# Performance work log

Measured on AMD Instinct MI355X. Metric: run time of the kernel, lower is better.

Reference implementation:

```python
import jax, jax.numpy as jnp
import numpy as np

N_ENVS = 8
MIN_SIGMA = 0.01

def setup_inputs() -> dict:
    key = jax.random.key(0)
    ks = jax.random.split(key, 16)
    B, T, d, L, H = 32, 64, 128, 64, 256
    H2 = H // 2
    s = 0.05
    return {
        "z_signal": jax.random.normal(ks[0], (B, T, d, L), dtype=jnp.float32),
        "z_corrupt": jax.random.normal(ks[1], (B, T, d, L), dtype=jnp.float32),
        "A": jax.random.uniform(ks[2], (d, d), dtype=jnp.float32),
        "regime": jax.random.randint(ks[3], (B,), 0, N_ENVS),
        # signal_proj: Linear(L -> H)
        "W_sig": jax.random.normal(ks[4], (L, H), dtype=jnp.float32) * s,
        "b_sig": jnp.zeros((H,), dtype=jnp.float32),
        # per-env mechanisms: Linear(H->H), ReLU, Linear(H->2), stacked over envs
        "W1e": jax.random.normal(ks[5], (N_ENVS, H, H), dtype=jnp.float32) * s,
        "b1e": jnp.zeros((N_ENVS, H), dtype=jnp.float32),
        "W2e": jax.random.normal(ks[6], (N_ENVS, H, 2), dtype=jnp.float32) * s,
        "b2e": jnp.zeros((N_ENVS, 2), dtype=jnp.float32),
        # corrupt path: Linear(L -> H//2), ReLU, Linear(H//2 -> 1)
        "Wc": jax.random.normal(ks[7], (L, H2), dtype=jnp.float32) * s,
        "bc": jnp.zeros((H2,), dtype=jnp.float32),
        "Wo": jax.random.normal(ks[8], (H2, 1), dtype=jnp.float32) * s,
        "bo": jnp.zeros((1,), dtype=jnp.float32),
    }

def reference(z_signal, z_corrupt, A, regime, W_sig, b_sig, W1e, b1e, W2e, b2e, Wc, bc, Wo, bo):
    # z_signal: [B,T,d,L], A: [d,d]
    # z_agg[b,t,i,l] = sum_j A[j,i] * z_signal[b,t,j,l]  (A^T @ z per slice)
    z_agg = jnp.einsum('ji,btjl->btil', A, z_signal)
    h_signal = jnp.einsum('btdl,lh->btdh', z_agg, W_sig) + b_sig  # [B,T,d,H]

    # env dispatch: e_idx = regime if regime < n_envs else 0 (per batch element)
    eidx = jnp.where(regime >= N_ENVS, 0, regime)
    W1 = W1e[eidx]  # [B,H,H]
    b1 = b1e[eidx]  # [B,H]
    W2 = W2e[eidx]  # [B,H,2]
    b2 = b2e[eidx]  # [B,2]

    h1 = jax.nn.relu(jnp.einsum('btdh,bhk->btdk', h_signal, W1) + b1[:, None, None, :])
    out = jnp.einsum('btdh,bhk->btdk', h1, W2) + b2[:, None, None, :]  # [B,T,d,2]
    mu = out[..., 0]
    sigma = jax.nn.softplus(out[..., 1]) + MIN_SIGMA

    # corrupt contribution
    h_c = jnp.einsum('btdl,lh->btdh', z_corrupt, Wc) + bc
    contrib = (jnp.einsum('btdh,ho->btdo', jax.nn.relu(h_c), Wo) + bo)[..., 0]  # [B,T,d]
    mu = mu + contrib
    return mu, sigma
```

## Files before the change

### kernel.cpp

```cpp
#include <hip/hip_runtime.h>


typedef __attribute__((ext_vector_type(8))) short short8;
typedef __attribute__((ext_vector_type(4))) float f32x4;

#define MFMA16(a, b, c) __builtin_amdgcn_mfma_f32_16x16x32_bf16((a), (b), (c), 0, 0, 0)

__device__ __forceinline__ unsigned short f2bf(float f) {
  union { float f; unsigned u; } v; v.f = f;
  unsigned r = v.u + 0x7fffu + ((v.u >> 16) & 1u);
  return (unsigned short)(r >> 16);
}

__device__ __forceinline__ void gload16(const void* gsrc, void* ldsdst) {
  __builtin_amdgcn_global_load_lds(
      (const __attribute__((address_space(1))) unsigned int*)gsrc,
      (__attribute__((address_space(3))) unsigned int*)ldsdst, 16, 0, 0);
}

__global__ void setup_k(const float* __restrict__ A, const float* __restrict__ W_sig,
                        const float* __restrict__ b_sig, const float* __restrict__ W1e,
                        const float* __restrict__ b1e, const float* __restrict__ W2e,
                        const float* __restrict__ Wc,
                        unsigned short* __restrict__ wsw1s, unsigned short* __restrict__ at_f,
                        unsigned short* __restrict__ wct_f, float* __restrict__ bw) {
  int blk = blockIdx.x, tid = threadIdx.x;
  if (blk < 512) {
    int e = blk >> 6, l = blk & 63, h = tid;
    const float* w1 = W1e + e * 65536 + h;
    const float* ws = W_sig + l * 256;
    float acc = 0.f;
    #pragma unroll 8
    for (int h1 = 0; h1 < 256; ++h1) acc = fmaf(ws[h1], w1[h1 * 256], acc);
    int c = h >> 7, hh = h & 127, gl = l >> 3, e8 = l & 7;
    wsw1s[((e * 2 + c) * 128 + hh) * 64 + ((gl ^ (hh & 7)) << 3) + e8] = f2bf(acc);
  } else if (blk < 576) {
    int idx = (blk - 512) * 256 + tid;
    int frag = idx >> 3, e8 = idx & 7;
    int it = frag >> 8, ks = (frag >> 6) & 3, lane = frag & 63;
    int j = ks * 32 + (lane >> 4) * 8 + e8, i = it * 16 + (lane & 15);
    at_f[idx] = f2bf(A[j * 128 + i]);
  } else if (blk < 608) {
    int idx = (blk - 576) * 256 + tid;
    int frag = idx >> 3, e8 = idx & 7;
    int ht = frag >> 7, ks = (frag >> 6) & 1, lane = frag & 63;
    int l = ks * 32 + (lane >> 4) * 8 + e8, h = ht * 16 + (lane & 15);
    wct_f[idx] = f2bf(Wc[l * 128 + h]);
  } else if (blk < 624) {
    int idx = (blk - 608) * 256 + tid;
    int e = idx >> 9, r = idx & 511;
    bw[e * 768 + 256 + r] = W2e[idx];
  } else {
    int e = blk - 624, h = tid;
    const float* w1 = W1e + e * 65536 + h;
    float acc = b1e[e * 256 + h];
    for (int h1 = 0; h1 < 256; ++h1) acc = fmaf(b_sig[h1], w1[h1 * 256], acc);
    bw[e * 768 + h] = acc;
  }
}

__global__ __launch_bounds__(256, 3) void dec_k(
    const float* __restrict__ zs, const float* __restrict__ zcr,
    const int* __restrict__ regime, const float* __restrict__ b2e,
    const float* __restrict__ bc, const float* __restrict__ Wo,
    const float* __restrict__ bo,
    const unsigned short* __restrict__ wsw1s, const unsigned short* __restrict__ at_f,
    const unsigned short* __restrict__ wct_f, const float* __restrict__ bw,
    float* __restrict__ out) {
  __shared__ __align__(16) char sm[54272];
  float* s_bias1 = (float*)(sm + 49152);
  float* s_W2    = s_bias1 + 256;
  float* s_cpart = (float*)(sm + 52224);

  const int bt = ((blockIdx.x & 7) << 8) | (blockIdx.x >> 3);
  const int tid = threadIdx.x;
  const int lane = tid & 63, wave = tid >> 6, lg = lane >> 4, l15 = lane & 15;
  int e = regime[bt >> 6]; if (e >= 8) e = 0;
  const float b2_0 = b2e[2 * e], b2_1 = b2e[2 * e + 1], bo0 = bo[0];

  const float* Z  = zs  + (size_t)bt * 8192;
  const float* Zc = zcr + (size_t)bt * 8192;
  const unsigned short* wse = wsw1s + (size_t)e * 16384;

  #pragma unroll
  for (int k = 0; k < 4; ++k)
    gload16((const char*)wse + (k * 256 + tid) * 16,
            sm + 32768 + (k * 256 + wave * 64) * 16);
  if (wave < 3)
    gload16((const char*)(bw + e * 768) + tid * 16, sm + 49152 + wave * 1024);

  float4 zcv[8];
  #pragma unroll
  for (int k = 0; k < 8; ++k) {
    int g = k * 256 + tid, d = g >> 4, l0 = (g & 15) * 4;
    zcv[k] = *(const float4*)(Zc + d * 64 + l0);
  }
  float4 z0v[4], z1v[4];
  #pragma unroll
  for (int k = 0; k < 4; ++k) {
    int g = k * 256 + tid, j = (g >> 4) * 2, l0 = (g & 15) * 4;
    const float* p = Z + j * 64 + l0;
    z0v[k] = *(const float4*)p;
    z1v[k] = *(const float4*)(p + 64);
  }
  short8 wfr[2][2];
  #pragma unroll
  for (int m = 0; m < 2; ++m)
    #pragma unroll
    for (int ks = 0; ks < 2; ++ks)
      wfr[m][ks] = *(const short8*)(wct_f + ((((wave * 2 + m) * 2 + ks) * 64 + lane) << 3));

  #pragma unroll
  for (int k = 0; k < 8; ++k) {
    int g = k * 256 + tid, d = g >> 4, l0 = (g & 15) * 4;
    unsigned lo = (unsigned)f2bf(zcv[k].x) | ((unsigned)f2bf(zcv[k].y) << 16);
    unsigned hi = (unsigned)f2bf(zcv[k].z) | ((unsigned)f2bf(zcv[k].w) << 16);
    int a = (d * 128 + l0 * 2) ^ ((d & 7) << 4);
    *(unsigned long long*)(sm + 16384 + a) = ((unsigned long long)hi << 32) | lo;
  }
  #pragma unroll
  for (int k = 0; k < 4; ++k) {
    int g = k * 256 + tid, j = (g >> 4) * 2, l0 = (g & 15) * 4;
    float a0[4] = {z0v[k].x, z0v[k].y, z0v[k].z, z0v[k].w};
    float a1[4] = {z1v[k].x, z1v[k].y, z1v[k].z, z1v[k].w};
    #pragma unroll
    for (int i2 = 0; i2 < 4; ++i2) {
      int l = l0 + i2;
      unsigned v = (unsigned)f2bf(a0[i2]) | ((unsigned)f2bf(a1[i2]) << 16);
      int a = (l * 256 + j * 2) ^ ((((l >> 2) ^ l) & 7) << 4);
      *(unsigned*)(sm + a) = v;
    }
  }
  __syncthreads();

  short8 abfr[2][4];
  #pragma unroll
  for (int m = 0; m < 2; ++m)
    #pragma unroll
    for (int ks = 0; ks < 4; ++ks)
      abfr[m][ks] = *(const short8*)(at_f + ((((wave * 2 + m) * 4 + ks) * 64 + lane) << 3));
  float4 bcv[2], wov[2];
  #pragma unroll
  for (int m = 0; m < 2; ++m) {
    int hb = (wave * 2 + m) * 16 + lg * 4;
    bcv[m] = *(const float4*)(bc + hb);
    wov[m] = *(const float4*)(Wo + hb);
  }

  float cp[8];
  #pragma unroll
  for (int dt = 0; dt < 8; ++dt) cp[dt] = 0.f;
  #pragma unroll
  for (int dt = 0; dt < 8; ++dt) {
    int brow = dt * 16 + l15;
    short8 bfr0 = *(const short8*)(sm + 16384 + ((brow * 128 + lg * 16) ^ ((brow & 7) << 4)));
    short8 bfr1 = *(const short8*)(sm + 16384 + ((brow * 128 + lg * 16 + 64) ^ ((brow & 7) << 4)));
    #pragma unroll
    for (int m = 0; m < 2; ++m) {
      f32x4 acc = (f32x4){0.f, 0.f, 0.f, 0.f};
      acc = MFMA16(wfr[m][0], bfr0, acc);
      acc = MFMA16(wfr[m][1], bfr1, acc);
      #pragma unroll
      for (int r = 0; r < 4; ++r)
        cp[dt] += fmaxf(acc[r] + bcv[m][r], 0.f) * wov[m][r];
    }
  }
  #pragma unroll
  for (int dt = 0; dt < 8; ++dt) {
    cp[dt] += __shfl_xor(cp[dt], 16);
    cp[dt] += __shfl_xor(cp[dt], 32);
  }
  if (lane < 16) {
    #pragma unroll
    for (int dt = 0; dt < 8; ++dt)
      s_cpart[wave * 128 + dt * 16 + lane] = cp[dt];
  }

  f32x4 acc1[4][2];
  #pragma unroll
  for (int lt = 0; lt < 4; ++lt)
    #pragma unroll
    for (int m = 0; m < 2; ++m) acc1[lt][m] = (f32x4){0.f, 0.f, 0.f, 0.f};
  #pragma unroll
  for (int ks = 0; ks < 4; ++ks) {
    #pragma unroll
    for (int lt = 0; lt < 4; ++lt) {
      int arow = lt * 16 + l15;
      short8 afr = *(const short8*)(sm + ((arow * 256 + lg * 16 + ks * 64) ^
                                          ((((arow >> 2) ^ arow) & 7) << 4)));
      #pragma unroll
      for (int m = 0; m < 2; ++m) acc1[lt][m] = MFMA16(afr, abfr[m][ks], acc1[lt][m]);
    }
  }
  __syncthreads();

  #pragma unroll
  for (int k = 0; k < 4; ++k)
    gload16((const char*)wse + 16384 + (k * 256 + tid) * 16,
            sm + (k * 256 + wave * 64) * 16);

  #pragma unroll
  for (int lt = 0; lt < 4; ++lt) {
    int l0 = lt * 16 + lg * 4;
    #pragma unroll
    for (int m = 0; m < 2; ++m) {
      int i = (wave * 2 + m) * 16 + l15;
      unsigned lo = (unsigned)f2bf(acc1[lt][m][0]) | ((unsigned)f2bf(acc1[lt][m][1]) << 16);
      unsigned hi = (unsigned)f2bf(acc1[lt][m][2]) | ((unsigned)f2bf(acc1[lt][m][3]) << 16);
      int a = (i * 128 + l0 * 2) ^ ((i & 7) << 4);
      *(unsigned long long*)(sm + 16384 + a) = ((unsigned long long)hi << 32) | lo;
    }
  }
  short8 mbfr[2][2];
  #pragma unroll
  for (int m = 0; m < 2; ++m) {
    int brow = (wave * 2 + m) * 16 + l15;
    #pragma unroll
    for (int ks = 0; ks < 2; ++ks)
      mbfr[m][ks] = *(const short8*)(sm + 16384 +
                       ((brow * 128 + lg * 16 + ks * 64) ^ ((brow & 7) << 4)));
  }

  float v0[2] = {0.f, 0.f}, v1[2] = {0.f, 0.f};
  #pragma unroll
  for (int c = 0; c < 2; ++c) {
    if (c == 1) __syncthreads();
    const char* wbase = (const char*)sm + (c == 0 ? 32768 : 0);
    #pragma unroll
    for (int ht = 0; ht < 8; ++ht) {
      int arow = ht * 16 + l15;
      int h4 = c * 128 + ht * 16 + lg * 4;
      short8 wa0 = *(const short8*)(wbase + ((arow * 128 + lg * 16) ^ ((arow & 7) << 4)));
      short8 wa1 = *(const short8*)(wbase + ((arow * 128 + lg * 16 + 64) ^ ((arow & 7) << 4)));
      float4 b1v = *(const float4*)(s_bias1 + h4);
      float4 w2a = *(const float4*)(s_W2 + h4 * 2);
      float4 w2b = *(const float4*)(s_W2 + h4 * 2 + 4);
      #pragma unroll
      for (int m = 0; m < 2; ++m) {
        f32x4 acc = (f32x4){0.f, 0.f, 0.f, 0.f};
        acc = MFMA16(wa0, mbfr[m][0], acc);
        acc = MFMA16(wa1, mbfr[m][1], acc);
        float p0 = fmaxf(acc[0] + b1v.x, 0.f), p1 = fmaxf(acc[1] + b1v.y, 0.f);
        float p2 = fmaxf(acc[2] + b1v.z, 0.f), p3 = fmaxf(acc[3] + b1v.w, 0.f);
        v0[m] = fmaf(p0, w2a.x, fmaf(p1, w2a.z, fmaf(p2, w2b.x, fmaf(p3, w2b.z, v0[m]))));
        v1[m] = fmaf(p0, w2a.y, fmaf(p1, w2a.w, fmaf(p2, w2b.y, fmaf(p3, w2b.w, v1[m]))));
      }
    }
  }
  #pragma unroll
  for (int m = 0; m < 2; ++m) {
    v0[m] += __shfl_xor(v0[m], 16); v0[m] += __shfl_xor(v0[m], 32);
    v1[m] += __shfl_xor(v1[m], 16); v1[m] += __shfl_xor(v1[m], 32);
  }
  if (lane < 16) {
    #pragma unroll
    for (int m = 0; m < 2; ++m) {
      int d = (wave * 2 + m) * 16 + lane;
      float contrib = s_cpart[d] + s_cpart[128 + d] + s_cpart[256 + d] + s_cpart[384 + d];
      float mu = v0[m] + b2_0 + bo0 + contrib;
      float x = v1[m] + b2_1;
      float sg = fmaxf(x, 0.f) + log1pf(expf(-fabsf(x))) + 0.01f;
      out[(size_t)bt * 128 + d] = mu;
      out[262144 + (size_t)bt * 128 + d] = sg;
    }
  }
}

extern "C" void kernel_launch(void* const* d_in, const int* in_sizes, int n_in,
                              void* d_out, int out_size, void* d_ws, size_t ws_size,
                              hipStream_t stream) {
  const float* zs    = (const float*)d_in[0];
  const float* zcr   = (const float*)d_in[1];
  const float* A     = (const float*)d_in[2];
  const int*   reg   = (const int*)d_in[3];
  const float* W_sig = (const float*)d_in[4];
  const float* b_sig = (const float*)d_in[5];
  const float* W1e   = (const float*)d_in[6];
  const float* b1e   = (const float*)d_in[7];
  const float* W2e   = (const float*)d_in[8];
  const float* b2e   = (const float*)d_in[9];
  const float* Wc    = (const float*)d_in[10];
  const float* bcp   = (const float*)d_in[11];
  const float* Wo    = (const float*)d_in[12];
  const float* bo    = (const float*)d_in[13];

  unsigned short* wsw1s = (unsigned short*)d_ws;
  unsigned short* at_f  = wsw1s + 131072;
  unsigned short* wct_f = at_f + 16384;
  float* bw             = (float*)(wct_f + 8192);

  setup_k<<<632, 256, 0, stream>>>(A, W_sig, b_sig, W1e, b1e, W2e, Wc,
                                   wsw1s, at_f, wct_f, bw);
  dec_k<<<2048, 256, 0, stream>>>(zs, zcr, reg, b2e, bcp, Wo, bo,
                                  wsw1s, at_f, wct_f, bw, (float*)d_out);
}
```

Before: 58.42 us.

## Load fused W_sig·W1 fragments directly into registers instead of LDS staging

```diff
diff --git a/kernel.cpp b/kernel.cpp
--- a/kernel.cpp
+++ b/kernel.cpp
@@ -1,4 +1,5 @@
 #include <hip/hip_runtime.h>
+#include <hip/hip_bf16.h>
 
 
 typedef __attribute__((ext_vector_type(8))) short short8;
@@ -12,6 +13,11 @@
   return (unsigned short)(r >> 16);
 }
 
+__device__ __forceinline__ unsigned pkbf(float a, float b) {
+  __hip_bfloat162 t = __float22bfloat162_rn(float2{a, b});
+  unsigned u; __builtin_memcpy(&u, &t, 4); return u;
+}
+
 __device__ __forceinline__ void gload16(const void* gsrc, void* ldsdst) {
   __builtin_amdgcn_global_load_lds(
       (const __attribute__((address_space(1))) unsigned int*)gsrc,
@@ -22,7 +28,7 @@
                         const float* __restrict__ b_sig, const float* __restrict__ W1e,
                         const float* __restrict__ b1e, const float* __restrict__ W2e,
                         const float* __restrict__ Wc,
-                        unsigned short* __restrict__ wsw1s, unsigned short* __restrict__ at_f,
+                        unsigned short* __restrict__ wsw1f, unsigned short* __restrict__ at_f,
                         unsigned short* __restrict__ wct_f, float* __restrict__ bw) {
   int blk = blockIdx.x, tid = threadIdx.x;
   if (blk < 512) {
@@ -32,8 +38,10 @@
     float acc = 0.f;
     #pragma unroll 8
     for (int h1 = 0; h1 < 256; ++h1) acc = fmaf(ws[h1], w1[h1 * 256], acc);
-    int c = h >> 7, hh = h & 127, gl = l >> 3, e8 = l & 7;
-    wsw1s[((e * 2 + c) * 128 + hh) * 64 + ((gl ^ (hh & 7)) << 3) + e8] = f2bf(acc);
+    int c = h >> 7, ht = (h >> 4) & 7, col = h & 15;
+    int kks = l >> 5, lgl = (l >> 3) & 3, e8 = l & 7;
+    int lane = lgl * 16 + col;
+    wsw1f[((((e * 2 + c) * 8 + ht) * 2 + kks) * 64 + lane) * 8 + e8] = f2bf(acc);
   } else if (blk < 576) {
     int idx = (blk - 512) * 256 + tid;
     int frag = idx >> 3, e8 = idx & 7;
@@ -59,18 +67,18 @@
   }
 }
 
-__global__ __launch_bounds__(256, 3) void dec_k(
+__global__ __launch_bounds__(256, 4) void dec_k(
     const float* __restrict__ zs, const float* __restrict__ zcr,
     const int* __restrict__ regime, const float* __restrict__ b2e,
     const float* __restrict__ bc, const float* __restrict__ Wo,
     const float* __restrict__ bo,
-    const unsigned short* __restrict__ wsw1s, const unsigned short* __restrict__ at_f,
+    const unsigned short* __restrict__ wsw1f, const unsigned short* __restrict__ at_f,
     const unsigned short* __restrict__ wct_f, const float* __restrict__ bw,
     float* __restrict__ out) {
-  __shared__ __align__(16) char sm[54272];
-  float* s_bias1 = (float*)(sm + 49152);
+  __shared__ __align__(16) char sm[37888];
+  float* s_bias1 = (float*)(sm + 32768);
   float* s_W2    = s_bias1 + 256;
-  float* s_cpart = (float*)(sm + 52224);
+  float* s_cpart = (float*)(sm + 35840);
 
   const int bt = ((blockIdx.x & 7) << 8) | (blockIdx.x >> 3);
   const int tid = threadIdx.x;
@@ -80,14 +88,9 @@
 
   const float* Z  = zs  + (size_t)bt * 8192;
   const float* Zc = zcr + (size_t)bt * 8192;
-  const unsigned short* wse = wsw1s + (size_t)e * 16384;
-
-  #pragma unroll
-  for (int k = 0; k < 4; ++k)
-    gload16((const char*)wse + (k * 256 + tid) * 16,
-            sm + 32768 + (k * 256 + wave * 64) * 16);
+
   if (wave < 3)
-    gload16((const char*)(bw + e * 768) + tid * 16, sm + 49152 + wave * 1024);
+    gload16((const char*)(bw + e * 768) + tid * 16, sm + 32768 + wave * 1024);
 
   float4 zcv[8];
   #pragma unroll
@@ -113,8 +116,8 @@
   #pragma unroll
   for (int k = 0; k < 8; ++k) {
     int g = k * 256 + tid, d = g >> 4, l0 = (g & 15) * 4;
-    unsigned lo = (unsigned)f2bf(zcv[k].x) | ((unsigned)f2bf(zcv[k].y) << 16);
-    unsigned hi = (unsigned)f2bf(zcv[k].z) | ((unsigned)f2bf(zcv[k].w) << 16);
+    unsigned lo = pkbf(zcv[k].x, zcv[k].y);
+    unsigned hi = pkbf(zcv[k].z, zcv[k].w);
     int a = (d * 128 + l0 * 2) ^ ((d & 7) << 4);
     *(unsigned long long*)(sm + 16384 + a) = ((unsigned long long)hi << 32) | lo;
   }
@@ -126,7 +129,7 @@
     #pragma unroll
     for (int i2 = 0; i2 < 4; ++i2) {
       int l = l0 + i2;
-      unsigned v = (unsigned)f2bf(a0[i2]) | ((unsigned)f2bf(a1[i2]) << 16);
+      unsigned v = pkbf(a0[i2], a1[i2]);
       int a = (l * 256 + j * 2) ^ ((((l >> 2) ^ l) & 7) << 4);
       *(unsigned*)(sm + a) = v;
     }
@@ -176,6 +179,14 @@
       s_cpart[wave * 128 + dt * 16 + lane] = cp[dt];
   }
 
+  const unsigned short* wse = wsw1f + (size_t)e * 16384;
+  short8 wsf0[8][2];
+  #pragma unroll
+  for (int ht = 0; ht < 8; ++ht)
+    #pragma unroll
+    for (int ks = 0; ks < 2; ++ks)
+      wsf0[ht][ks] = *(const short8*)(wse + (((ht * 2 + ks) * 64 + lane) << 3));
+
   f32x4 acc1[4][2];
   #pragma unroll
   for (int lt = 0; lt < 4; ++lt)
@@ -194,10 +205,12 @@
   }
   __syncthreads();
 
-  #pragma unroll
-  for (int k = 0; k < 4; ++k)
-    gload16((const char*)wse + 16384 + (k * 256 + tid) * 16,
-            sm + (k * 256 + wave * 64) * 16);
+  short8 wsf1[8][2];
+  #pragma unroll
+  for (int ht = 0; ht < 8; ++ht)
+    #pragma unroll
+    for (int ks = 0; ks < 2; ++ks)
+      wsf1[ht][ks] = *(const short8*)(wse + 8192 + (((ht * 2 + ks) * 64 + lane) << 3));
 
   #pragma unroll
   for (int lt = 0; lt < 4; ++lt) {
@@ -205,8 +218,8 @@
     #pragma unroll
     for (int m = 0; m < 2; ++m) {
       int i = (wave * 2 + m) * 16 + l15;
-      unsigned lo = (unsigned)f2bf(acc1[lt][m][0]) | ((unsigned)f2bf(acc1[lt][m][1]) << 16);
-      unsigned hi = (unsigned)f2bf(acc1[lt][m][2]) | ((unsigned)f2bf(acc1[lt][m][3]) << 16);
+      unsigned lo = pkbf(acc1[lt][m][0], acc1[lt][m][1]);
+      unsigned hi = pkbf(acc1[lt][m][2], acc1[lt][m][3]);
       int a = (i * 128 + l0 * 2) ^ ((i & 7) << 4);
       *(unsigned long long*)(sm + 16384 + a) = ((unsigned long long)hi << 32) | lo;
     }
@@ -224,22 +237,22 @@
   float v0[2] = {0.f, 0.f}, v1[2] = {0.f, 0.f};
   #pragma unroll
   for (int c = 0; c < 2; ++c) {
-    if (c == 1) __syncthreads();
-    const char* wbase = (const char*)sm + (c == 0 ? 32768 : 0);
     #pragma unroll
     for (int ht = 0; ht < 8; ++ht) {
-      int arow = ht * 16 + l15;
       int h4 = c * 128 + ht * 16 + lg * 4;
-      short8 wa0 = *(const short8*)(wbase + ((arow * 128 + lg * 16) ^ ((arow & 7) << 4)));
-      short8 wa1 = *(const short8*)(wbase + ((arow * 128 + lg * 16 + 64) ^ ((arow & 7) << 4)));
       float4 b1v = *(const float4*)(s_bias1 + h4);
       float4 w2a = *(const float4*)(s_W2 + h4 * 2);
       float4 w2b = *(const float4*)(s_W2 + h4 * 2 + 4);
       #pragma unroll
       for (int m = 0; m < 2; ++m) {
         f32x4 acc = (f32x4){0.f, 0.f, 0.f, 0.f};
-        acc = MFMA16(wa0, mbfr[m][0], acc);
-        acc = MFMA16(wa1, mbfr[m][1], acc);
+        if (c == 0) {
+          acc = MFMA16(wsf0[ht][0], mbfr[m][0], acc);
+          acc = MFMA16(wsf0[ht][1], mbfr[m][1], acc);
+        } else {
+          acc = MFMA16(wsf1[ht][0], mbfr[m][0], acc);
+          acc = MFMA16(wsf1[ht][1], mbfr[m][1], acc);
+        }
         float p0 = fmaxf(acc[0] + b1v.x, 0.f), p1 = fmaxf(acc[1] + b1v.y, 0.f);
         float p2 = fmaxf(acc[2] + b1v.z, 0.f), p3 = fmaxf(acc[3] + b1v.w, 0.f);
         v0[m] = fmaf(p0, w2a.x, fmaf(p1, w2a.z, fmaf(p2, w2b.x, fmaf(p3, w2b.z, v0[m]))));
@@ -284,13 +297,13 @@
   const float* Wo    = (const float*)d_in[12];
   const float* bo    = (const float*)d_in[13];
 
-  unsigned short* wsw1s = (unsigned short*)d_ws;
-  unsigned short* at_f  = wsw1s + 131072;
+  unsigned short* wsw1f = (unsigned short*)d_ws;
+  unsigned short* at_f  = wsw1f + 131072;
   unsigned short* wct_f = at_f + 16384;
   float* bw             = (float*)(wct_f + 8192);
 
   setup_k<<<632, 256, 0, stream>>>(A, W_sig, b_sig, W1e, b1e, W2e, Wc,
-                                   wsw1s, at_f, wct_f, bw);
+                                   wsw1f, at_f, wct_f, bw);
   dec_k<<<2048, 256, 0, stream>>>(zs, zcr, reg, b2e, bcp, Wo, bo,
-                                  wsw1s, at_f, wct_f, bw, (float*)d_out);
-}
+                                  wsw1f, at_f, wct_f, bw, (float*)d_out);
+}
```

Measured after the change: 51.96 us. 11.1% less time.
